# Performance work log

Measured on AMD Instinct MI355X. Metric: run time of the kernel, lower is better.

Reference implementation:

```python
import jax, jax.numpy as jnp
import numpy as np

CLAMP_MIN = -10.0
CLAMP_MAX = 10.0
B = 8
N = 100_000
EDGES = 3_200_000


def setup_inputs() -> dict:
    key = jax.random.key(0)
    ks = jax.random.split(key, 9)
    chem_influence = jax.random.normal(ks[0], (B, N), dtype=jnp.float32)
    E = jax.random.normal(ks[1], (B, N), dtype=jnp.float32)
    O = jax.random.normal(ks[2], (B, N), dtype=jnp.float32)
    src = jax.random.randint(ks[3], (EDGES,), 0, N, dtype=jnp.int64) if jax.config.jax_enable_x64 else jax.random.randint(ks[3], (EDGES,), 0, N).astype(jnp.int32)
    dst = jax.random.randint(ks[4], (EDGES,), 0, N).astype(src.dtype)
    w = jax.random.normal(ks[5], (EDGES,), dtype=jnp.float32)
    o_pre = jax.random.normal(ks[6], (B, N), dtype=jnp.float32)
    # learned per-neuron params (rnd_init=True ranges from the module)
    threshold = jax.random.uniform(ks[7], (N,), minval=-1.0, maxval=2.0, dtype=jnp.float32)
    decay = jax.random.uniform(ks[8], (N,), minval=0.05, maxval=1.0, dtype=jnp.float32)
    return {"chem_influence": chem_influence, "E": E, "O": O, "src": src,
            "dst": dst, "w": w, "o_pre": o_pre, "threshold": threshold, "decay": decay}


def reference(chem_influence, E, O, src, dst, w, o_pre, threshold, decay):
    # Gap-junction path: gather presyn output Oj and postsyn internal state En per edge
    Oj = o_pre[:, src]                    # (B, E)
    En = E[:, dst]                        # (B, E)
    contrib = Oj * w * jnp.sign(Oj - En)  # sign(Oj - En) * w_j * Oj
    # scatter-add edge contributions into the chemical-influence buffer (dup indices accumulate)
    chem = chem_influence.at[:, dst].add(contrib)  # (B, N)
    # Neuron dynamics (eqs 10, 11)
    S = jnp.clip(E + chem, CLAMP_MIN, CLAMP_MAX)
    gt = S > threshold
    mask = (~gt) & (S == E)
    new_o = jax.nn.relu(S - threshold)
    new_e = jnp.where(gt, new_o, jnp.where(mask, E - decay, S))
    # torch module returns (new_o, (new_e, new_o)); flatten the state tuple
    return new_o, new_e
```

## Files before the change

kernel.cpp:

```cpp
#include <hip/hip_runtime.h>

#define CLAMP_MIN_F (-10.0f)
#define CLAMP_MAX_F (10.0f)
#define BATCH 8
#define SUP_LOG 8
#define SNODES 256
#define MAXS 512
#define ESTR 9
#define EPB 16384
#define CH 2048
#define TB_BIN 1024
#define MAX4K 4096

__global__ void prep_o_kernel(const float* __restrict__ o_pre,
                              float* __restrict__ o_preT,
                              unsigned* __restrict__ total,
                              int N) {
    int n = blockIdx.x * blockDim.x + threadIdx.x;
    if (n < MAX4K) total[n] = 0u;
    if (n >= N) return;
    float o[BATCH];
    #pragma unroll
    for (int b = 0; b < BATCH; ++b) o[b] = o_pre[b * N + n];
    float4* op = (float4*)&o_preT[(size_t)n * BATCH];
    op[0] = make_float4(o[0], o[1], o[2], o[3]);
    op[1] = make_float4(o[4], o[5], o[6], o[7]);
}

__global__ __launch_bounds__(TB_BIN)
void hist_reserve_kernel(const int* __restrict__ dst,
                         unsigned* __restrict__ superTotal,
                         unsigned* __restrict__ offs0s,
                         int edges) {
    __shared__ unsigned sh[MAXS];
    int bid = blockIdx.x, tid = threadIdx.x;
    for (int s = tid; s < MAXS; s += blockDim.x) sh[s] = 0u;
    __syncthreads();
    int start = bid * EPB;
    int endE = min(edges, start + EPB);
    for (int i = start + tid; i < endE; i += blockDim.x)
        atomicAdd(&sh[((unsigned)dst[i]) >> SUP_LOG], 1u);
    __syncthreads();
    for (int s = tid; s < MAXS; s += blockDim.x) {
        unsigned c = sh[s];
        offs0s[(size_t)bid * MAXS + s] = c ? atomicAdd(&superTotal[s], c) : 0u;
    }
}

__global__ void scan4_kernel(const unsigned* __restrict__ total,
                             unsigned* __restrict__ base,
                             int KPAD) {
    __shared__ unsigned s1[1024];
    __shared__ unsigned s2[1024];
    int t = threadIdx.x;
    unsigned v0 = (4 * t     < KPAD) ? total[4 * t]     : 0u;
    unsigned v1 = (4 * t + 1 < KPAD) ? total[4 * t + 1] : 0u;
    unsigned v2 = (4 * t + 2 < KPAD) ? total[4 * t + 2] : 0u;
    unsigned v3 = (4 * t + 3 < KPAD) ? total[4 * t + 3] : 0u;
    unsigned sum = v0 + v1 + v2 + v3;
    s1[t] = sum;
    __syncthreads();
    unsigned* cur = s1;
    unsigned* nxt = s2;
    for (int off = 1; off < 1024; off <<= 1) {
        unsigned x = cur[t];
        if (t >= off) x += cur[t - off];
        __syncthreads();
        nxt[t] = x;
        __syncthreads();
        unsigned* tmp = cur; cur = nxt; nxt = tmp;
    }
    unsigned incl = cur[t];
    unsigned excl = incl - sum;
    base[4 * t]     = excl;
    base[4 * t + 1] = excl + v0;
    base[4 * t + 2] = excl + v0 + v1;
    base[4 * t + 3] = excl + v0 + v1 + v2;
    if (t == 1023) base[MAX4K] = incl;
}

__global__ __launch_bounds__(TB_BIN)
void scatter_kernel(const int* __restrict__ src,
                    const int* __restrict__ dst,
                    const float* __restrict__ w,
                    const unsigned* __restrict__ offs0s,
                    const unsigned* __restrict__ baseS,
                    int2* __restrict__ recS,
                    int edges) {
    __shared__ int2 srec[CH];
    __shared__ unsigned short ssup[CH];
    __shared__ unsigned cnt[MAXS];
    __shared__ unsigned sstart[MAXS];
    __shared__ unsigned cursor[MAXS];
    __shared__ unsigned pa[MAXS];
    __shared__ unsigned pb[MAXS];
    int bid = blockIdx.x, tid = threadIdx.x;
    for (int s = tid; s < MAXS; s += blockDim.x)
        cursor[s] = baseS[s] + offs0s[(size_t)bid * MAXS + s];
    int start = bid * EPB;
    int endE = min(edges, start + EPB);
    for (int cs = start; cs < endE; cs += CH) {
        int m = min(CH, endE - cs);
        __syncthreads();
        for (int s = tid; s < MAXS; s += blockDim.x) cnt[s] = 0u;
        __syncthreads();
        int2 hrec[2]; unsigned hsup[2], hpos[2]; bool hv[2];
        #pragma unroll
        for (int j = 0; j < 2; ++j) {
            int i = tid + j * TB_BIN;
            hv[j] = (i < m);
            if (hv[j]) {
                int gi = cs + i;
                int d = dst[gi];
                unsigned key = (((unsigned)d & (SNODES - 1)) << 17) | (unsigned)src[gi];
                hrec[j] = make_int2((int)key, __float_as_int(w[gi]));
                hsup[j] = (unsigned)d >> SUP_LOG;
                hpos[j] = atomicAdd(&cnt[hsup[j]], 1u);
            }
        }
        __syncthreads();
        {
            unsigned* cur = pa;
            unsigned* nxt = pb;
            if (tid < MAXS) cur[tid] = cnt[tid];
            __syncthreads();
            for (int off = 1; off < MAXS; off <<= 1) {
                unsigned v = 0;
                if (tid < MAXS) { v = cur[tid]; if (tid >= off) v += cur[tid - off]; }
                __syncthreads();
                if (tid < MAXS) nxt[tid] = v;
                __syncthreads();
                unsigned* t2 = cur; cur = nxt; nxt = t2;
            }
            if (tid < MAXS) sstart[tid] = cur[tid] - cnt[tid];
            __syncthreads();
        }
        #pragma unroll
        for (int j = 0; j < 2; ++j) {
            if (hv[j]) {
                unsigned idx = sstart[hsup[j]] + hpos[j];
                srec[idx] = hrec[j];
                ssup[idx] = (unsigned short)hsup[j];
            }
        }
        __syncthreads();
        #pragma unroll
        for (int j = 0; j < 2; ++j) {
            int i = tid + j * TB_BIN;
            if (i < m) {
                unsigned sup = ssup[i];
                unsigned gpos = cursor[sup] + ((unsigned)i - sstart[sup]);
                recS[gpos] = srec[i];
            }
        }
        __syncthreads();
        for (int s = tid; s < MAXS; s += blockDim.x) cursor[s] += cnt[s];
    }
}

__global__ __launch_bounds__(TB_BIN)
void accum_kernel(const int2* __restrict__ recS,
                  const unsigned* __restrict__ baseS,
                  const float* __restrict__ o_preT,
                  const float* __restrict__ E,
                  const float* __restrict__ chem_in,
                  const float* __restrict__ thr,
                  const float* __restrict__ decay,
                  float* __restrict__ new_o,
                  float* __restrict__ new_e,
                  int N) {
    __shared__ int2 srec[CH];
    __shared__ float e_lds[SNODES * ESTR];
    __shared__ float acc_st[SNODES * ESTR];
    __shared__ unsigned cnt[SNODES];
    __shared__ unsigned sstart[SNODES];
    __shared__ unsigned pa[SNODES];
    __shared__ unsigned pb[SNODES];
    int sb = blockIdx.x;
    int ns = sb << SUP_LOG;
    int cntn = min(SNODES, N - ns);
    int tid = threadIdx.x;

    for (int i = tid; i < SNODES * BATCH; i += blockDim.x) {
        int b = i >> SUP_LOG;
        int n = i & (SNODES - 1);
        if (n < cntn) e_lds[n * ESTR + b] = E[(size_t)b * N + ns + n];
    }
    __syncthreads();

    int b = tid & 7;
    int g = tid >> 3;
    float En0 = e_lds[g * ESTR + b];
    float En1 = e_lds[(g + 128) * ESTR + b];
    float acc0 = 0.f, acc1 = 0.f;

    unsigned r0 = baseS[sb], r1 = baseS[sb + 1];
    for (unsigned cs = r0; cs < r1; cs += CH) {
        unsigned m = min((unsigned)CH, r1 - cs);
        for (int s = tid; s < SNODES; s += blockDim.x) cnt[s] = 0u;
        __syncthreads();
        int2 hrec[2]; unsigned hdl[2], hpos[2]; bool hv[2];
        #pragma unroll
        for (int j = 0; j < 2; ++j) {
            unsigned i = (unsigned)tid + (unsigned)j * TB_BIN;
            hv[j] = (i < m);
            if (hv[j]) {
                int2 rec = recS[cs + i];
                unsigned dl = ((unsigned)rec.x >> 17) & (SNODES - 1);
                hrec[j] = rec;
                hdl[j] = dl;
                hpos[j] = atomicAdd(&cnt[dl], 1u);
            }
        }
        __syncthreads();
        {
            unsigned* cur = pa;
            unsigned* nxt = pb;
            if (tid < SNODES) cur[tid] = cnt[tid];
            __syncthreads();
            for (int off = 1; off < SNODES; off <<= 1) {
                unsigned v = 0;
                if (tid < SNODES) { v = cur[tid]; if (tid >= off) v += cur[tid - off]; }
                __syncthreads();
                if (tid < SNODES) nxt[tid] = v;
                __syncthreads();
                unsigned* t2 = cur; cur = nxt; nxt = t2;
            }
            if (tid < SNODES) sstart[tid] = cur[tid] - cnt[tid];
            __syncthreads();
        }
        #pragma unroll
        for (int j = 0; j < 2; ++j)
            if (hv[j]) srec[sstart[hdl[j]] + hpos[j]] = hrec[j];
        __syncthreads();
        {
            unsigned st = sstart[g], en = st + cnt[g];
            for (unsigned r = st; r < en; ++r) {
                int2 rec = srec[r];
                unsigned si = (unsigned)rec.x & 0x1FFFFu;
                float Oj = o_preT[((size_t)si << 3) + b];
                float wv = __int_as_float(rec.y);
                float df = Oj - En0;
                float sg = (df > 0.f) ? 1.f : ((df < 0.f) ? -1.f : 0.f);
                acc0 += Oj * wv * sg;
            }
        }
        {
            unsigned st = sstart[g + 128], en = st + cnt[g + 128];
            for (unsigned r = st; r < en; ++r) {
                int2 rec = srec[r];
                unsigned si = (unsigned)rec.x & 0x1FFFFu;
                float Oj = o_preT[((size_t)si << 3) + b];
                float wv = __int_as_float(rec.y);
                float df = Oj - En1;
                float sg = (df > 0.f) ? 1.f : ((df < 0.f) ? -1.f : 0.f);
                acc1 += Oj * wv * sg;
            }
        }
        __syncthreads();
    }

    acc_st[g * ESTR + b] = acc0;
    acc_st[(g + 128) * ESTR + b] = acc1;
    __syncthreads();

    for (int i = tid; i < SNODES * BATCH; i += blockDim.x) {
        int bb = i >> SUP_LOG;
        int n = i & (SNODES - 1);
        if (n >= cntn) continue;
        float e = e_lds[n * ESTR + bb];
        float S = e + chem_in[(size_t)bb * N + ns + n] + acc_st[n * ESTR + bb];
        S = fminf(fmaxf(S, CLAMP_MIN_F), CLAMP_MAX_F);
        float t  = thr[ns + n];
        float dc = decay[ns + n];
        bool gt = S > t;
        float no = fmaxf(S - t, 0.f);
        float ne = gt ? no : ((S == e) ? (e - dc) : S);
        new_o[(size_t)bb * N + ns + n] = no;
        new_e[(size_t)bb * N + ns + n] = ne;
    }
}

__global__ void prep_kernel(const float* __restrict__ chem_in,
                            const float* __restrict__ o_pre,
                            const float* __restrict__ E,
                            float* __restrict__ chemT,
                            float* __restrict__ o_preT,
                            float* __restrict__ E_T,
                            int N) {
    int n = blockIdx.x * blockDim.x + threadIdx.x;
    if (n >= N) return;
    float c[BATCH], o[BATCH], ee[BATCH];
    #pragma unroll
    for (int b = 0; b < BATCH; ++b) {
        c[b]  = chem_in[b * N + n];
        o[b]  = o_pre[b * N + n];
        ee[b] = E[b * N + n];
    }
    float4* cp = (float4*)&chemT[(size_t)n * BATCH];
    cp[0] = make_float4(c[0], c[1], c[2], c[3]);
    cp[1] = make_float4(c[4], c[5], c[6], c[7]);
    float4* op = (float4*)&o_preT[(size_t)n * BATCH];
    op[0] = make_float4(o[0], o[1], o[2], o[3]);
    op[1] = make_float4(o[4], o[5], o[6], o[7]);
    float4* ep = (float4*)&E_T[(size_t)n * BATCH];
    ep[0] = make_float4(ee[0], ee[1], ee[2], ee[3]);
    ep[1] = make_float4(ee[4], ee[5], ee[6], ee[7]);
}
__global__ void edge_scatter_eb(const int* __restrict__ src,
                                const int* __restrict__ dst,
                                const float* __restrict__ w,
                                const float* __restrict__ o_preT,
                                const float* __restrict__ E_T,
                                float* __restrict__ chemT,
                                int edges) {
    int t = blockIdx.x * blockDim.x + threadIdx.x;
    int e = t >> 3;
    int b = t & 7;
    if (e >= edges) return;
    int s = src[e]; int d = dst[e]; float we = w[e];
    float Oj = o_preT[(size_t)s * BATCH + b];
    float En = E_T[(size_t)d * BATCH + b];
    float diff = Oj - En;
    float sg = (diff > 0.0f) ? 1.0f : ((diff < 0.0f) ? -1.0f : 0.0f);
    atomicAdd(&chemT[(size_t)d * BATCH + b], Oj * we * sg);
}
__global__ void finalize_nb(const float* __restrict__ E,
                            const float* __restrict__ chemT,
                            const float* __restrict__ thr,
                            const float* __restrict__ decay,
                            float* __restrict__ new_o,
                            float* __restrict__ new_e, int N) {
    int n = blockIdx.x * blockDim.x + threadIdx.x;
    if (n >= N) return;
    const float4* cp = (const float4*)&chemT[(size_t)n * BATCH];
    float4 c0 = cp[0], c1 = cp[1];
    float c[BATCH] = {c0.x, c0.y, c0.z, c0.w, c1.x, c1.y, c1.z, c1.w};
    float t = thr[n];
    float dc = decay[n];
    #pragma unroll
    for (int b = 0; b < BATCH; ++b) {
        int i = b * N + n;
        float e = E[i];
        float S = fminf(fmaxf(e + c[b], CLAMP_MIN_F), CLAMP_MAX_F);
        bool gt = S > t;
        float no = fmaxf(S - t, 0.0f);
        float ne = gt ? no : ((S == e) ? (e - dc) : S);
        new_o[i] = no;
        new_e[i] = ne;
    }
}

static inline size_t align256(size_t x) { return (x + 255) & ~(size_t)255; }

extern "C" void kernel_launch(void* const* d_in, const int* in_sizes, int n_in,
                              void* d_out, int out_size, void* d_ws, size_t ws_size,
                              hipStream_t stream) {
    const float* chem_influence = (const float*)d_in[0];
    const float* E              = (const float*)d_in[1];
    const int*   src            = (const int*)d_in[3];
    const int*   dst            = (const int*)d_in[4];
    const float* w              = (const float*)d_in[5];
    const float* o_pre          = (const float*)d_in[6];
    const float* threshold      = (const float*)d_in[7];
    const float* decay          = (const float*)d_in[8];

    const int edges = in_sizes[3];
    const int BN    = in_sizes[0];
    const int N     = in_sizes[7];

    float* new_o = (float*)d_out;
    float* new_e = (float*)d_out + BN;

    const int TB = 256;
    int nblk = (N + TB - 1) / TB;

    const int NS = (N + SNODES - 1) >> SUP_LOG;
    const int NB = (edges + EPB - 1) / EPB;

    size_t off = 0;
    size_t opreT_off  = off; off += align256((size_t)BN * 4);
    size_t base_off   = off; off += align256((size_t)(MAX4K + 1) * 4);
    size_t total_off  = off; off += align256((size_t)MAX4K * 4);
    size_t offs0_off  = off; off += align256((size_t)NB * MAXS * 4);
    size_t rec_off    = off; off += align256((size_t)edges * 8);
    size_t need = off;

    char* wsb = (char*)d_ws;

    if (NS <= MAXS && N <= (1 << 17) && ws_size >= need) {
        float*    o_preT = (float*)(wsb + opreT_off);
        unsigned* baseS  = (unsigned*)(wsb + base_off);
        unsigned* total  = (unsigned*)(wsb + total_off);
        unsigned* offs0s = (unsigned*)(wsb + offs0_off);
        int2*     recS   = (int2*)(wsb + rec_off);

        prep_o_kernel<<<nblk, TB, 0, stream>>>(o_pre, o_preT, total, N);
        hist_reserve_kernel<<<NB, TB_BIN, 0, stream>>>(dst, total, offs0s, edges);
        scan4_kernel<<<1, 1024, 0, stream>>>(total, baseS, MAXS);
        scatter_kernel<<<NB, TB_BIN, 0, stream>>>(src, dst, w, offs0s, baseS,
                                                  recS, edges);
        accum_kernel<<<NS, TB_BIN, 0, stream>>>(recS, baseS, o_preT, E,
                                                chem_influence, threshold, decay,
                                                new_o, new_e, N);
    } else if (ws_size >= 3 * (size_t)BN * 4) {
        float* chemT  = (float*)d_ws;
        float* o_preT = chemT + BN;
        float* E_T    = o_preT + BN;
        prep_kernel<<<nblk, TB, 0, stream>>>(chem_influence, o_pre, E,
                                             chemT, o_preT, E_T, N);
        long long ethreads = (long long)edges * BATCH;
        int gblk = (int)((ethreads + TB - 1) / TB);
        edge_scatter_eb<<<gblk, TB, 0, stream>>>(src, dst, w, o_preT, E_T,
                                                 chemT, edges);
        finalize_nb<<<nblk, TB, 0, stream>>>(E, chemT, threshold, decay,
                                             new_o, new_e, N);
    }
}
```

Measured before the change: 96.37 us.

## Balance accum work by fixed edge windows with run-length LDS atomics

The accumulation kernel now gives each 8-thread group a fixed contiguous window of sorted edge records instead of two destination nodes. This is meant to remove load imbalance from skewed per-node degrees. Each group sums runs of equal destinations and flushes them with LDS atomicAdd into a shared accumulator. The block size drops from 1024 to 512 threads, with four records loaded per thread. The 256-entry Hillis-Steele scan is replaced by a single-wavefront shuffle scan. Float atomics make the summation order nondeterministic, and the per-edge E lookup now comes from LDS.

```diff
diff --git a/kernel.cpp b/kernel.cpp
--- a/kernel.cpp
+++ b/kernel.cpp
@@ -10,6 +10,8 @@
 #define EPB 16384
 #define CH 2048
 #define TB_BIN 1024
+#define TB_ACC 512
+#define WIN (CH / (TB_ACC / 8))
 #define MAX4K 4096
 
 __global__ void prep_o_kernel(const float* __restrict__ o_pre,
@@ -158,7 +160,7 @@
     }
 }
 
-__global__ __launch_bounds__(TB_BIN)
+__global__ __launch_bounds__(TB_ACC)
 void accum_kernel(const int2* __restrict__ recS,
                   const unsigned* __restrict__ baseS,
                   const float* __restrict__ o_preT,
@@ -171,16 +173,15 @@
                   int N) {
     __shared__ int2 srec[CH];
     __shared__ float e_lds[SNODES * ESTR];
-    __shared__ float acc_st[SNODES * ESTR];
+    __shared__ float acc_lds[SNODES * ESTR];
     __shared__ unsigned cnt[SNODES];
     __shared__ unsigned sstart[SNODES];
-    __shared__ unsigned pa[SNODES];
-    __shared__ unsigned pb[SNODES];
     int sb = blockIdx.x;
     int ns = sb << SUP_LOG;
     int cntn = min(SNODES, N - ns);
     int tid = threadIdx.x;
 
+    for (int i = tid; i < SNODES * ESTR; i += blockDim.x) acc_lds[i] = 0.f;
     for (int i = tid; i < SNODES * BATCH; i += blockDim.x) {
         int b = i >> SUP_LOG;
         int n = i & (SNODES - 1);
@@ -190,19 +191,15 @@
 
     int b = tid & 7;
     int g = tid >> 3;
-    float En0 = e_lds[g * ESTR + b];
-    float En1 = e_lds[(g + 128) * ESTR + b];
-    float acc0 = 0.f, acc1 = 0.f;
-
     unsigned r0 = baseS[sb], r1 = baseS[sb + 1];
     for (unsigned cs = r0; cs < r1; cs += CH) {
         unsigned m = min((unsigned)CH, r1 - cs);
-        for (int s = tid; s < SNODES; s += blockDim.x) cnt[s] = 0u;
-        __syncthreads();
-        int2 hrec[2]; unsigned hdl[2], hpos[2]; bool hv[2];
+        if (tid < SNODES) cnt[tid] = 0u;
+        __syncthreads();
+        int2 hrec[4]; unsigned hdl[4], hpos[4]; bool hv[4];
         #pragma unroll
-        for (int j = 0; j < 2; ++j) {
-            unsigned i = (unsigned)tid + (unsigned)j * TB_BIN;
+        for (int j = 0; j < 4; ++j) {
+            unsigned i = (unsigned)tid + (unsigned)j * TB_ACC;
             hv[j] = (i < m);
             if (hv[j]) {
                 int2 rec = recS[cs + i];
@@ -213,55 +210,52 @@
             }
         }
         __syncthreads();
-        {
-            unsigned* cur = pa;
-            unsigned* nxt = pb;
-            if (tid < SNODES) cur[tid] = cnt[tid];
-            __syncthreads();
-            for (int off = 1; off < SNODES; off <<= 1) {
-                unsigned v = 0;
-                if (tid < SNODES) { v = cur[tid]; if (tid >= off) v += cur[tid - off]; }
-                __syncthreads();
-                if (tid < SNODES) nxt[tid] = v;
-                __syncthreads();
-                unsigned* t2 = cur; cur = nxt; nxt = t2;
-            }
-            if (tid < SNODES) sstart[tid] = cur[tid] - cnt[tid];
-            __syncthreads();
-        }
+        if (tid < 64) {
+            unsigned v0 = cnt[4 * tid], v1 = cnt[4 * tid + 1];
+            unsigned v2 = cnt[4 * tid + 2], v3 = cnt[4 * tid + 3];
+            unsigned s = v0 + v1 + v2 + v3;
+            unsigned inc = s;
+            #pragma unroll
+            for (int off = 1; off < 64; off <<= 1) {
+                unsigned t2 = __shfl_up(inc, off, 64);
+                if (tid >= off) inc += t2;
+            }
+            unsigned excl = inc - s;
+            sstart[4 * tid]     = excl;
+            sstart[4 * tid + 1] = excl + v0;
+            sstart[4 * tid + 2] = excl + v0 + v1;
+            sstart[4 * tid + 3] = excl + v0 + v1 + v2;
+        }
+        __syncthreads();
         #pragma unroll
-        for (int j = 0; j < 2; ++j)
+        for (int j = 0; j < 4; ++j)
             if (hv[j]) srec[sstart[hdl[j]] + hpos[j]] = hrec[j];
         __syncthreads();
-        {
-            unsigned st = sstart[g], en = st + cnt[g];
-            for (unsigned r = st; r < en; ++r) {
-                int2 rec = srec[r];
-                unsigned si = (unsigned)rec.x & 0x1FFFFu;
-                float Oj = o_preT[((size_t)si << 3) + b];
-                float wv = __int_as_float(rec.y);
-                float df = Oj - En0;
-                float sg = (df > 0.f) ? 1.f : ((df < 0.f) ? -1.f : 0.f);
-                acc0 += Oj * wv * sg;
-            }
-        }
-        {
-            unsigned st = sstart[g + 128], en = st + cnt[g + 128];
-            for (unsigned r = st; r < en; ++r) {
-                int2 rec = srec[r];
-                unsigned si = (unsigned)rec.x & 0x1FFFFu;
-                float Oj = o_preT[((size_t)si << 3) + b];
-                float wv = __int_as_float(rec.y);
-                float df = Oj - En1;
-                float sg = (df > 0.f) ? 1.f : ((df < 0.f) ? -1.f : 0.f);
-                acc1 += Oj * wv * sg;
-            }
-        }
-        __syncthreads();
-    }
-
-    acc_st[g * ESTR + b] = acc0;
-    acc_st[(g + 128) * ESTR + b] = acc1;
+        unsigned lo = (unsigned)g * WIN;
+        unsigned hi = min(m, lo + (unsigned)WIN);
+        int curn = -1;
+        float accv = 0.f;
+        for (unsigned r = lo; r < hi; ++r) {
+            int2 rec = srec[r];
+            unsigned dl = ((unsigned)rec.x >> 17) & (SNODES - 1);
+            unsigned si = (unsigned)rec.x & 0x1FFFFu;
+            float Oj = o_preT[((size_t)si << 3) + b];
+            float wv = __int_as_float(rec.y);
+            float En = e_lds[dl * ESTR + b];
+            float df = Oj - En;
+            float sg = (df > 0.f) ? 1.f : ((df < 0.f) ? -1.f : 0.f);
+            float contrib = Oj * wv * sg;
+            if ((int)dl != curn) {
+                if (curn >= 0) atomicAdd(&acc_lds[curn * ESTR + b], accv);
+                curn = (int)dl;
+                accv = contrib;
+            } else {
+                accv += contrib;
+            }
+        }
+        if (curn >= 0) atomicAdd(&acc_lds[curn * ESTR + b], accv);
+        __syncthreads();
+    }
     __syncthreads();
 
     for (int i = tid; i < SNODES * BATCH; i += blockDim.x) {
@@ -269,7 +263,7 @@
         int n = i & (SNODES - 1);
         if (n >= cntn) continue;
         float e = e_lds[n * ESTR + bb];
-        float S = e + chem_in[(size_t)bb * N + ns + n] + acc_st[n * ESTR + bb];
+        float S = e + chem_in[(size_t)bb * N + ns + n] + acc_lds[n * ESTR + bb];
         S = fminf(fmaxf(S, CLAMP_MIN_F), CLAMP_MAX_F);
         float t  = thr[ns + n];
         float dc = decay[ns + n];
@@ -400,7 +394,7 @@
         scan4_kernel<<<1, 1024, 0, stream>>>(total, baseS, MAXS);
         scatter_kernel<<<NB, TB_BIN, 0, stream>>>(src, dst, w, offs0s, baseS,
                                                   recS, edges);
-        accum_kernel<<<NS, TB_BIN, 0, stream>>>(recS, baseS, o_preT, E,
+        accum_kernel<<<NS, TB_ACC, 0, stream>>>(recS, baseS, o_preT, E,
                                                 chem_influence, threshold, decay,
                                                 new_o, new_e, N);
     } else if (ws_size >= 3 * (size_t)BN * 4) {
```

After: 128.3 us (median of 2 runs). +33.1%, slower.

## Add second-level fine binning so accumulation runs on 32-node blocks

Applied to the files above, without the earlier changes.

Replaces the single 256-node superbin pass with a two-level radix partition. A fine 4096-bin histogram is summed per column and scanned. Edges are first scattered into superbins, then re-scattered into 32-node fine bins with ballot-based local ranking. The accumulation kernel then runs one 256-thread block per 32-node group. The goal is more, smaller accumulation blocks for better occupancy and load balance, and a cheaper per-chunk local sort with fewer barriers. The cost is an extra full read and write of the edge record array and two extra kernel launches.

```diff
diff --git a/kernel.cpp b/kernel.cpp
--- a/kernel.cpp
+++ b/kernel.cpp
@@ -6,7 +6,9 @@
 #define SUP_LOG 8
 #define SNODES 256
 #define MAXS 512
-#define ESTR 9
+#define FIN_LOG 5
+#define FNODES 32
+#define ASTR 9
 #define EPB 16384
 #define CH 2048
 #define TB_BIN 1024
@@ -14,10 +16,10 @@
 
 __global__ void prep_o_kernel(const float* __restrict__ o_pre,
                               float* __restrict__ o_preT,
-                              unsigned* __restrict__ total,
+                              unsigned* __restrict__ superTotal,
                               int N) {
     int n = blockIdx.x * blockDim.x + threadIdx.x;
-    if (n < MAX4K) total[n] = 0u;
+    if (n < MAXS) superTotal[n] = 0u;
     if (n >= N) return;
     float o[BATCH];
     #pragma unroll
@@ -28,23 +30,50 @@
 }
 
 __global__ __launch_bounds__(TB_BIN)
-void hist_reserve_kernel(const int* __restrict__ dst,
-                         unsigned* __restrict__ superTotal,
-                         unsigned* __restrict__ offs0s,
-                         int edges) {
-    __shared__ unsigned sh[MAXS];
+void hist_fine_kernel(const int* __restrict__ dst,
+                      unsigned* __restrict__ superTotal,
+                      unsigned* __restrict__ histRows,
+                      unsigned* __restrict__ offs0s,
+                      int edges) {
+    __shared__ unsigned shf[MAX4K];
     int bid = blockIdx.x, tid = threadIdx.x;
-    for (int s = tid; s < MAXS; s += blockDim.x) sh[s] = 0u;
+    for (int k = tid; k < MAX4K; k += blockDim.x) shf[k] = 0u;
     __syncthreads();
     int start = bid * EPB;
     int endE = min(edges, start + EPB);
     for (int i = start + tid; i < endE; i += blockDim.x)
-        atomicAdd(&sh[((unsigned)dst[i]) >> SUP_LOG], 1u);
+        atomicAdd(&shf[((unsigned)dst[i]) >> FIN_LOG], 1u);
     __syncthreads();
+    for (int k = tid; k < MAX4K; k += blockDim.x)
+        histRows[(size_t)bid * MAX4K + k] = shf[k];
     for (int s = tid; s < MAXS; s += blockDim.x) {
-        unsigned c = sh[s];
+        unsigned c = 0;
+        #pragma unroll
+        for (int j = 0; j < 8; ++j) c += shf[8 * s + j];
         offs0s[(size_t)bid * MAXS + s] = c ? atomicAdd(&superTotal[s], c) : 0u;
     }
+}
+
+__global__ void colsum_kernel(const unsigned* __restrict__ histRows,
+                              unsigned* __restrict__ fineTotal,
+                              int NB) {
+    int k = blockIdx.x * blockDim.x + threadIdx.x;
+    if (k >= MAX4K) return;
+    unsigned s = 0;
+    int b = 0;
+    for (; b + 8 <= NB; b += 8) {
+        unsigned v0 = histRows[(size_t)(b + 0) * MAX4K + k];
+        unsigned v1 = histRows[(size_t)(b + 1) * MAX4K + k];
+        unsigned v2 = histRows[(size_t)(b + 2) * MAX4K + k];
+        unsigned v3 = histRows[(size_t)(b + 3) * MAX4K + k];
+        unsigned v4 = histRows[(size_t)(b + 4) * MAX4K + k];
+        unsigned v5 = histRows[(size_t)(b + 5) * MAX4K + k];
+        unsigned v6 = histRows[(size_t)(b + 6) * MAX4K + k];
+        unsigned v7 = histRows[(size_t)(b + 7) * MAX4K + k];
+        s += v0 + v1 + v2 + v3 + v4 + v5 + v6 + v7;
+    }
+    for (; b < NB; ++b) s += histRows[(size_t)b * MAX4K + k];
+    fineTotal[k] = s;
 }
 
 __global__ void scan4_kernel(const unsigned* __restrict__ total,
@@ -80,13 +109,13 @@
 }
 
 __global__ __launch_bounds__(TB_BIN)
-void scatter_kernel(const int* __restrict__ src,
-                    const int* __restrict__ dst,
-                    const float* __restrict__ w,
-                    const unsigned* __restrict__ offs0s,
-                    const unsigned* __restrict__ baseS,
-                    int2* __restrict__ recS,
-                    int edges) {
+void scatter1_kernel(const int* __restrict__ src,
+                     const int* __restrict__ dst,
+                     const float* __restrict__ w,
+                     const unsigned* __restrict__ offs0s,
+                     const unsigned* __restrict__ fineBase,
+                     int2* __restrict__ recS,
+                     int edges) {
     __shared__ int2 srec[CH];
     __shared__ unsigned short ssup[CH];
     __shared__ unsigned cnt[MAXS];
@@ -96,7 +125,7 @@
     __shared__ unsigned pb[MAXS];
     int bid = blockIdx.x, tid = threadIdx.x;
     for (int s = tid; s < MAXS; s += blockDim.x)
-        cursor[s] = baseS[s] + offs0s[(size_t)bid * MAXS + s];
+        cursor[s] = fineBase[8 * s] + offs0s[(size_t)bid * MAXS + s];
     int start = bid * EPB;
     int endE = min(edges, start + EPB);
     for (int cs = start; cs < endE; cs += CH) {
@@ -159,117 +188,170 @@
 }
 
 __global__ __launch_bounds__(TB_BIN)
-void accum_kernel(const int2* __restrict__ recS,
-                  const unsigned* __restrict__ baseS,
-                  const float* __restrict__ o_preT,
-                  const float* __restrict__ E,
-                  const float* __restrict__ chem_in,
-                  const float* __restrict__ thr,
-                  const float* __restrict__ decay,
-                  float* __restrict__ new_o,
-                  float* __restrict__ new_e,
-                  int N) {
+void scatter2_kernel(const int2* __restrict__ recS,
+                     const unsigned* __restrict__ fineBase,
+                     int2* __restrict__ recS2) {
     __shared__ int2 srec[CH];
-    __shared__ float e_lds[SNODES * ESTR];
-    __shared__ float acc_st[SNODES * ESTR];
-    __shared__ unsigned cnt[SNODES];
-    __shared__ unsigned sstart[SNODES];
-    __shared__ unsigned pa[SNODES];
-    __shared__ unsigned pb[SNODES];
-    int sb = blockIdx.x;
-    int ns = sb << SUP_LOG;
-    int cntn = min(SNODES, N - ns);
-    int tid = threadIdx.x;
-
-    for (int i = tid; i < SNODES * BATCH; i += blockDim.x) {
-        int b = i >> SUP_LOG;
-        int n = i & (SNODES - 1);
-        if (n < cntn) e_lds[n * ESTR + b] = E[(size_t)b * N + ns + n];
-    }
+    __shared__ unsigned char sfin[CH];
+    __shared__ unsigned cnt8[8];
+    __shared__ unsigned sstart8[9];
+    __shared__ unsigned fineRun[8];
+    int sb = blockIdx.x, tid = threadIdx.x;
+    int lane = tid & 63;
+    if (tid < 8) fineRun[tid] = fineBase[8 * sb + tid];
+    unsigned r0 = fineBase[8 * sb];
+    unsigned r1 = fineBase[8 * sb + 8];
     __syncthreads();
-
-    int b = tid & 7;
-    int g = tid >> 3;
-    float En0 = e_lds[g * ESTR + b];
-    float En1 = e_lds[(g + 128) * ESTR + b];
-    float acc0 = 0.f, acc1 = 0.f;
-
-    unsigned r0 = baseS[sb], r1 = baseS[sb + 1];
     for (unsigned cs = r0; cs < r1; cs += CH) {
         unsigned m = min((unsigned)CH, r1 - cs);
-        for (int s = tid; s < SNODES; s += blockDim.x) cnt[s] = 0u;
-        __syncthreads();
-        int2 hrec[2]; unsigned hdl[2], hpos[2]; bool hv[2];
+        if (tid < 8) cnt8[tid] = 0u;
+        __syncthreads();
+        int2 hrec[2]; unsigned hf[2], hpos[2]; bool hv[2];
         #pragma unroll
         for (int j = 0; j < 2; ++j) {
             unsigned i = (unsigned)tid + (unsigned)j * TB_BIN;
             hv[j] = (i < m);
+            unsigned f = 8;
             if (hv[j]) {
-                int2 rec = recS[cs + i];
-                unsigned dl = ((unsigned)rec.x >> 17) & (SNODES - 1);
+                hrec[j] = recS[cs + i];
+                f = (((unsigned)hrec[j].x >> 17) >> FIN_LOG) & 7;
+            }
+            hf[j] = f;
+            for (unsigned ff = 0; ff < 8; ++ff) {
+                unsigned long long mk = __ballot(f == ff);
+                if (f == ff) {
+                    int leader = (int)(__ffsll((long long)mk) - 1);
+                    unsigned base = 0;
+                    if (lane == leader)
+                        base = atomicAdd(&cnt8[ff], (unsigned)__popcll(mk));
+                    base = __shfl(base, leader, 64);
+                    unsigned myoff = (unsigned)__popcll(mk & ((1ULL << lane) - 1ULL));
+                    hpos[j] = base + myoff;
+                }
+            }
+        }
+        __syncthreads();
+        if (tid == 0) {
+            unsigned run = 0;
+            #pragma unroll
+            for (int fq = 0; fq < 8; ++fq) { sstart8[fq] = run; run += cnt8[fq]; }
+            sstart8[8] = run;
+        }
+        __syncthreads();
+        #pragma unroll
+        for (int j = 0; j < 2; ++j) {
+            if (hv[j]) {
+                unsigned idx = sstart8[hf[j]] + hpos[j];
+                srec[idx] = hrec[j];
+                sfin[idx] = (unsigned char)hf[j];
+            }
+        }
+        __syncthreads();
+        #pragma unroll
+        for (int j = 0; j < 2; ++j) {
+            unsigned i = (unsigned)tid + (unsigned)j * TB_BIN;
+            if (i < m) {
+                unsigned f = sfin[i];
+                recS2[fineRun[f] + (i - sstart8[f])] = srec[i];
+            }
+        }
+        __syncthreads();
+        if (tid < 8) fineRun[tid] += cnt8[tid];
+    }
+}
+
+__global__ __launch_bounds__(256)
+void accum12_kernel(const int2* __restrict__ recS2,
+                    const unsigned* __restrict__ fineBase,
+                    const float* __restrict__ o_preT,
+                    const float* __restrict__ E,
+                    const float* __restrict__ chem_in,
+                    const float* __restrict__ thr,
+                    const float* __restrict__ decay,
+                    float* __restrict__ new_o,
+                    float* __restrict__ new_e,
+                    int N) {
+    __shared__ int2 srec[CH];
+    __shared__ float e_lds[FNODES * ASTR];
+    __shared__ float acc_st[FNODES * ASTR];
+    __shared__ unsigned cnt[FNODES];
+    __shared__ unsigned sstart[FNODES + 1];
+    int k = blockIdx.x;
+    int ns = k << FIN_LOG;
+    int cnt_n = min(FNODES, N - ns);
+    int tid = threadIdx.x;
+
+    for (int i = tid; i < FNODES * BATCH; i += blockDim.x) {
+        int b = i >> FIN_LOG;
+        int n = i & (FNODES - 1);
+        if (n < cnt_n) e_lds[n * ASTR + b] = E[(size_t)b * N + ns + n];
+    }
+    __syncthreads();
+
+    int b = tid & 7;
+    int g = tid >> 3;
+    float En = e_lds[g * ASTR + b];
+    float accv = 0.f;
+
+    unsigned b0 = fineBase[k], b1 = fineBase[k + 1];
+    for (unsigned cs = b0; cs < b1; cs += CH) {
+        unsigned m = min((unsigned)CH, b1 - cs);
+        if (tid < FNODES) cnt[tid] = 0u;
+        __syncthreads();
+        int2 hrec[8]; unsigned hmeta[8];
+        #pragma unroll
+        for (int j = 0; j < 8; ++j) {
+            unsigned i = (unsigned)tid + (unsigned)j * 256u;
+            if (i < m) {
+                int2 rec = recS2[cs + i];
+                unsigned dl = ((unsigned)rec.x >> 17) & (FNODES - 1);
+                unsigned pos = atomicAdd(&cnt[dl], 1u);
                 hrec[j] = rec;
-                hdl[j] = dl;
-                hpos[j] = atomicAdd(&cnt[dl], 1u);
-            }
-        }
-        __syncthreads();
-        {
-            unsigned* cur = pa;
-            unsigned* nxt = pb;
-            if (tid < SNODES) cur[tid] = cnt[tid];
-            __syncthreads();
-            for (int off = 1; off < SNODES; off <<= 1) {
-                unsigned v = 0;
-                if (tid < SNODES) { v = cur[tid]; if (tid >= off) v += cur[tid - off]; }
-                __syncthreads();
-                if (tid < SNODES) nxt[tid] = v;
-                __syncthreads();
-                unsigned* t2 = cur; cur = nxt; nxt = t2;
-            }
-            if (tid < SNODES) sstart[tid] = cur[tid] - cnt[tid];
-            __syncthreads();
-        }
-        #pragma unroll
-        for (int j = 0; j < 2; ++j)
-            if (hv[j]) srec[sstart[hdl[j]] + hpos[j]] = hrec[j];
-        __syncthreads();
-        {
-            unsigned st = sstart[g], en = st + cnt[g];
-            for (unsigned r = st; r < en; ++r) {
-                int2 rec = srec[r];
-                unsigned si = (unsigned)rec.x & 0x1FFFFu;
-                float Oj = o_preT[((size_t)si << 3) + b];
-                float wv = __int_as_float(rec.y);
-                float df = Oj - En0;
-                float sg = (df > 0.f) ? 1.f : ((df < 0.f) ? -1.f : 0.f);
-                acc0 += Oj * wv * sg;
-            }
-        }
-        {
-            unsigned st = sstart[g + 128], en = st + cnt[g + 128];
-            for (unsigned r = st; r < en; ++r) {
-                int2 rec = srec[r];
-                unsigned si = (unsigned)rec.x & 0x1FFFFu;
-                float Oj = o_preT[((size_t)si << 3) + b];
-                float wv = __int_as_float(rec.y);
-                float df = Oj - En1;
-                float sg = (df > 0.f) ? 1.f : ((df < 0.f) ? -1.f : 0.f);
-                acc1 += Oj * wv * sg;
-            }
-        }
-        __syncthreads();
-    }
-
-    acc_st[g * ESTR + b] = acc0;
-    acc_st[(g + 128) * ESTR + b] = acc1;
+                hmeta[j] = (dl << 16) | pos;
+            } else {
+                hmeta[j] = 0xFFFFFFFFu;
+            }
+        }
+        __syncthreads();
+        if (tid == 0) {
+            unsigned run = 0;
+            #pragma unroll
+            for (int d = 0; d < FNODES; ++d) { sstart[d] = run; run += cnt[d]; }
+            sstart[FNODES] = run;
+        }
+        __syncthreads();
+        #pragma unroll
+        for (int j = 0; j < 8; ++j) {
+            if (hmeta[j] != 0xFFFFFFFFu) {
+                unsigned dl = hmeta[j] >> 16;
+                unsigned pos = hmeta[j] & 0xFFFFu;
+                srec[sstart[dl] + pos] = hrec[j];
+            }
+        }
+        __syncthreads();
+        unsigned st = sstart[g];
+        unsigned en = st + cnt[g];
+        for (unsigned r = st; r < en; ++r) {
+            int2 rec = srec[r];
+            unsigned si = (unsigned)rec.x & 0x1FFFFu;
+            float Oj = o_preT[((size_t)si << 3) + b];
+            float wv = __int_as_float(rec.y);
+            float df = Oj - En;
+            float sg = (df > 0.f) ? 1.f : ((df < 0.f) ? -1.f : 0.f);
+            accv += Oj * wv * sg;
+        }
+        __syncthreads();
+    }
+
+    acc_st[g * ASTR + b] = accv;
     __syncthreads();
 
-    for (int i = tid; i < SNODES * BATCH; i += blockDim.x) {
-        int bb = i >> SUP_LOG;
-        int n = i & (SNODES - 1);
-        if (n >= cntn) continue;
-        float e = e_lds[n * ESTR + bb];
-        float S = e + chem_in[(size_t)bb * N + ns + n] + acc_st[n * ESTR + bb];
+    for (int i = tid; i < FNODES * BATCH; i += blockDim.x) {
+        int bb = i >> FIN_LOG;
+        int n = i & (FNODES - 1);
+        if (n >= cnt_n) continue;
+        float e = e_lds[n * ASTR + bb];
+        float S = e + chem_in[(size_t)bb * N + ns + n] + acc_st[n * ASTR + bb];
         S = fminf(fmaxf(S, CLAMP_MIN_F), CLAMP_MAX_F);
         float t  = thr[ns + n];
         float dc = decay[ns + n];
@@ -376,33 +458,43 @@
     int nblk = (N + TB - 1) / TB;
 
     const int NS = (N + SNODES - 1) >> SUP_LOG;
+    const int KF = (N + FNODES - 1) >> FIN_LOG;
     const int NB = (edges + EPB - 1) / EPB;
 
     size_t off = 0;
     size_t opreT_off  = off; off += align256((size_t)BN * 4);
-    size_t base_off   = off; off += align256((size_t)(MAX4K + 1) * 4);
-    size_t total_off  = off; off += align256((size_t)MAX4K * 4);
+    size_t fbase_off  = off; off += align256((size_t)(MAX4K + 1) * 4);
+    size_t ftot_off   = off; off += align256((size_t)MAX4K * 4);
+    size_t stot_off   = off; off += align256((size_t)MAXS * 4);
+    size_t hist_off   = off; off += align256((size_t)NB * MAX4K * 4);
     size_t offs0_off  = off; off += align256((size_t)NB * MAXS * 4);
     size_t rec_off    = off; off += align256((size_t)edges * 8);
+    size_t rec2_off   = off; off += align256((size_t)edges * 8);
     size_t need = off;
 
     char* wsb = (char*)d_ws;
 
-    if (NS <= MAXS && N <= (1 << 17) && ws_size >= need) {
-        float*    o_preT = (float*)(wsb + opreT_off);
-        unsigned* baseS  = (unsigned*)(wsb + base_off);
-        unsigned* total  = (unsigned*)(wsb + total_off);
-        unsigned* offs0s = (unsigned*)(wsb + offs0_off);
-        int2*     recS   = (int2*)(wsb + rec_off);
-
-        prep_o_kernel<<<nblk, TB, 0, stream>>>(o_pre, o_preT, total, N);
-        hist_reserve_kernel<<<NB, TB_BIN, 0, stream>>>(dst, total, offs0s, edges);
-        scan4_kernel<<<1, 1024, 0, stream>>>(total, baseS, MAXS);
-        scatter_kernel<<<NB, TB_BIN, 0, stream>>>(src, dst, w, offs0s, baseS,
-                                                  recS, edges);
-        accum_kernel<<<NS, TB_BIN, 0, stream>>>(recS, baseS, o_preT, E,
-                                                chem_influence, threshold, decay,
-                                                new_o, new_e, N);
+    if (NS <= MAXS && KF <= MAX4K - 1 && N <= (1 << 17) && ws_size >= need) {
+        float*    o_preT   = (float*)(wsb + opreT_off);
+        unsigned* fineBase = (unsigned*)(wsb + fbase_off);
+        unsigned* fineTot  = (unsigned*)(wsb + ftot_off);
+        unsigned* supTot   = (unsigned*)(wsb + stot_off);
+        unsigned* histRows = (unsigned*)(wsb + hist_off);
+        unsigned* offs0s   = (unsigned*)(wsb + offs0_off);
+        int2*     recS     = (int2*)(wsb + rec_off);
+        int2*     recS2    = (int2*)(wsb + rec2_off);
+
+        prep_o_kernel<<<nblk, TB, 0, stream>>>(o_pre, o_preT, supTot, N);
+        hist_fine_kernel<<<NB, TB_BIN, 0, stream>>>(dst, supTot, histRows,
+                                                    offs0s, edges);
+        colsum_kernel<<<MAX4K / TB, TB, 0, stream>>>(histRows, fineTot, NB);
+        scan4_kernel<<<1, 1024, 0, stream>>>(fineTot, fineBase, MAX4K);
+        scatter1_kernel<<<NB, TB_BIN, 0, stream>>>(src, dst, w, offs0s,
+                                                   fineBase, recS, edges);
+        scatter2_kernel<<<NS, TB_BIN, 0, stream>>>(recS, fineBase, recS2);
+        accum12_kernel<<<KF, 256, 0, stream>>>(recS2, fineBase, o_preT, E,
+                                               chem_influence, threshold, decay,
+                                               new_o, new_e, N);
     } else if (ws_size >= 3 * (size_t)BN * 4) {
         float* chemT  = (float*)d_ws;
         float* o_preT = chemT + BN;
```

Result: slower. 116.0 us (+20.4%).
